# Optimization experiments

Measured on AMD Instinct MI355X. Metric: run time of the kernel, lower is better.

Reference implementation:

```python
import jax, jax.numpy as jnp
import numpy as np

EPS = 1e-8
BETA = 0.05
K = 8192
D = 256
M = 32768


def _l2_normalize(x, axis=-1):
    # matches torch F.normalize: x / max(||x||, eps)
    n = jnp.linalg.norm(x, axis=axis, keepdims=True)
    return x / jnp.maximum(n, EPS)


def setup_inputs() -> dict:
    key = jax.random.key(0)
    kz, ke = jax.random.split(key)
    z = jax.random.normal(kz, (M, D), dtype=jnp.float32)
    # codebook initialized as unit-norm rows, as in the torch __init__
    E = _l2_normalize(jax.random.normal(ke, (K, D), dtype=jnp.float32), axis=1)
    return {"z": z, "E": E}


def reference(z, E):
    z_flat = z.reshape(-1, z.shape[-1])          # [M, D]
    z_n = _l2_normalize(z_flat, axis=1)          # [M, D]
    E_n = _l2_normalize(E, axis=1)               # [K, D]
    sims = jnp.einsum('md,kd->mk', z_n, E_n)     # [M, K] cosine similarity
    idx = jnp.argmax(sims, axis=1)               # [M]
    zq = E[idx]                                  # [M, D] gather
    zq_n = _l2_normalize(zq, axis=1)
    commit = jnp.mean((jax.lax.stop_gradient(zq_n) - z_n) ** 2)
    codebk = jnp.mean((zq_n - jax.lax.stop_gradient(z_n)) ** 2)
    loss = commit + BETA * codebk
    zq_st = z_flat + jax.lax.stop_gradient(zq - z_flat)  # straight-through
    return loss, zq_st, idx
```

## Files before the change

kernel.cpp:

```cpp
#include <hip/hip_runtime.h>
#include <float.h>
#include <math.h>
#include <stdint.h>

#define M_ROWS 32768
#define K_CODES 8192
#define DDIM 256
#define BM 64
#define BN 64
#define NTILES (K_CODES / BN)
#define DELTA 0.009f
#define CAP 16
#define FLAGBIT 0x10000

typedef __attribute__((ext_vector_type(8))) short short8;
typedef __attribute__((ext_vector_type(4))) float f32x4;

__device__ inline unsigned short f2bf(float f) {
    unsigned u = __float_as_uint(f);
    return (unsigned short)((u + 0x7fffu + ((u >> 16) & 1u)) >> 16);
}
__device__ inline unsigned fkey(float f) {
    unsigned u = __float_as_uint(f);
    return u ^ ((unsigned)((int)u >> 31) | 0x80000000u);
}
__device__ inline float fkey_inv(unsigned k) {
    unsigned u = (k & 0x80000000u) ? (k ^ 0x80000000u) : ~k;
    return __uint_as_float(u);
}

#define GLOAD16(gsrc, ldst)                                                     \
    __builtin_amdgcn_global_load_lds(                                           \
        (const __attribute__((address_space(1))) void*)(gsrc),                  \
        (__attribute__((address_space(3))) void*)(ldst), 16, 0, 0)

__global__ __launch_bounds__(256) void k_norm_E(const float* __restrict__ E,
                                                float* __restrict__ En,
                                                unsigned short* __restrict__ En_b) {
    int wid  = threadIdx.x >> 6;
    int lane = threadIdx.x & 63;
    int row  = blockIdx.x * 4 + wid;
    const float* e = E + (size_t)row * DDIM;
    float v[4];
    float ssq = 0.f;
#pragma unroll
    for (int p = 0; p < 4; ++p) { v[p] = e[lane + 64 * p]; ssq += v[p] * v[p]; }
#pragma unroll
    for (int off = 32; off >= 1; off >>= 1) ssq += __shfl_xor(ssq, off);
    float inv = 1.f / fmaxf(sqrtf(ssq), 1e-8f);
    float* o = En + (size_t)row * DDIM;
    unsigned short* ob = En_b + (size_t)row * DDIM;
#pragma unroll
    for (int p = 0; p < 4; ++p) {
        float nv = v[p] * inv;
        o[lane + 64 * p]  = nv;
        ob[lane + 64 * p] = f2bf(nv);
    }
}

__global__ __launch_bounds__(256, 2) void k_cand(
    const float* __restrict__ z,
    const unsigned short* __restrict__ En_b,
    unsigned char* __restrict__ cand_cnt,
    int* __restrict__ cand_k) {

    __shared__ __attribute__((aligned(16))) char smem[65536];
    unsigned* rowmaxKey = (unsigned*)smem;
    int*      cnt       = (int*)(smem + 256);
    int*      list      = (int*)(smem + 512);

    const int tid  = threadIdx.x;
    const int lane = tid & 63;
    const int wid  = tid >> 6;
    const int lo   = lane & 15;
    const int hi   = lane >> 4;
    const int m0   = blockIdx.x * BM;

    const char* eb = (const char*)En_b;
    char* b0 = smem + wid * 16384;
    char* b1 = smem + wid * 16384 + 8192;

    int sofs[8];
#pragma unroll
    for (int i = 0; i < 8; ++i) {
        int G   = i * 64 + lane;
        int row = G >> 5;
        int g   = (G & 31) ^ (row & 7);
        sofs[i] = (wid * 16 + row) * 512 + g * 16;
    }

    auto stage = [&](int ktile, char* bufp) {
        const char* tb = eb + (size_t)ktile * (BN * 512);
#pragma unroll
        for (int i = 0; i < 8; ++i)
            GLOAD16(tb + sofs[i], bufp + i * 1024);
    };

    stage(0, b0);
    stage(1, b1);

    short8 af[4][8];
#pragma unroll
    for (int mi = 0; mi < 4; ++mi) {
        const float* zr = z + (size_t)(m0 + mi * 16 + lo) * DDIM;
        float ssq = 0.f;
#pragma unroll
        for (int ks = 0; ks < 8; ++ks) {
            int e0 = (ks * 4 + hi) * 8;
            float4 a = *(const float4*)&zr[e0];
            float4 b = *(const float4*)&zr[e0 + 4];
            ssq += a.x * a.x + a.y * a.y + a.z * a.z + a.w * a.w;
            ssq += b.x * b.x + b.y * b.y + b.z * b.z + b.w * b.w;
        }
        ssq += __shfl_xor(ssq, 16);
        ssq += __shfl_xor(ssq, 32);
        float inv = 1.f / fmaxf(sqrtf(ssq), 1e-8f);
        const float* zr2 = zr;
        asm volatile("" : "+v"(zr2));
#pragma unroll
        for (int ks = 0; ks < 8; ++ks) {
            int e0 = (ks * 4 + hi) * 8;
            float4 a = *(const float4*)&zr2[e0];
            float4 b = *(const float4*)&zr2[e0 + 4];
            short8 s8;
            s8[0] = (short)f2bf(a.x * inv); s8[1] = (short)f2bf(a.y * inv);
            s8[2] = (short)f2bf(a.z * inv); s8[3] = (short)f2bf(a.w * inv);
            s8[4] = (short)f2bf(b.x * inv); s8[5] = (short)f2bf(b.y * inv);
            s8[6] = (short)f2bf(b.z * inv); s8[7] = (short)f2bf(b.w * inv);
            af[mi][ks] = s8;
        }
    }

    float v1[16], v2[16];
    int   k1[16];
#pragma unroll
    for (int s = 0; s < 16; ++s) { v1[s] = -FLT_MAX; v2[s] = -FLT_MAX; k1[s] = 0; }

    __syncthreads();

    const int bswz = lo & 7;

    for (int t = 0; t < NTILES; ++t) {
        if (t < NTILES - 1) asm volatile("s_waitcnt vmcnt(8)" ::: "memory");
        else                asm volatile("s_waitcnt vmcnt(0)" ::: "memory");
        __builtin_amdgcn_sched_barrier(0);

        const unsigned short* Bc = (const unsigned short*)((t & 1) ? b1 : b0);
        f32x4 acc[4];
#pragma unroll
        for (int mi = 0; mi < 4; ++mi) acc[mi] = (f32x4){0.f, 0.f, 0.f, 0.f};
#pragma unroll
        for (int ks = 0; ks < 8; ++ks) {
            short8 bf = *(const short8*)&Bc[lo * 256 + (((ks * 4 + hi) ^ bswz)) * 8];
#pragma unroll
            for (int mi = 0; mi < 4; ++mi)
                acc[mi] = __builtin_amdgcn_mfma_f32_16x16x32_bf16(af[mi][ks], bf, acc[mi], 0, 0, 0);
        }

        const int kv = t * BN + wid * 16 + lo;
#pragma unroll
        for (int mi = 0; mi < 4; ++mi)
#pragma unroll
            for (int r = 0; r < 4; ++r) {
                int s = mi * 4 + r;
                float v = acc[mi][r];
                v2[s] = fmaxf(v2[s], fminf(v1[s], v));
                k1[s] = (v > v1[s]) ? kv : k1[s];
                v1[s] = fmaxf(v1[s], v);
            }

        if (t + 2 < NTILES) {
            asm volatile("s_waitcnt lgkmcnt(0)" ::: "memory");
            __builtin_amdgcn_sched_barrier(0);
            stage(t + 2, (t & 1) ? b1 : b0);
        }
    }

    __syncthreads();
    if (tid < BM) { cnt[tid] = 0; rowmaxKey[tid] = 0u; }
    __syncthreads();

#pragma unroll
    for (int s = 0; s < 16; ++s) {
        float w = v1[s];
        w = fmaxf(w, __shfl_xor(w, 1));
        w = fmaxf(w, __shfl_xor(w, 2));
        w = fmaxf(w, __shfl_xor(w, 4));
        w = fmaxf(w, __shfl_xor(w, 8));
        if (lo == 0) {
            int row = (s >> 2) * 16 + hi * 4 + (s & 3);
            atomicMax(&rowmaxKey[row], fkey(w));
        }
    }
    __syncthreads();

#pragma unroll
    for (int s = 0; s < 16; ++s) {
        int row = (s >> 2) * 16 + hi * 4 + (s & 3);
        float thr = fkey_inv(rowmaxKey[row]) - DELTA;
        if (v1[s] >= thr) {
            int pos = atomicAdd(&cnt[row], 1);
            if (pos < CAP) list[row * CAP + pos] = k1[s];
        }
        if (v2[s] >= thr) {
            int pos = atomicAdd(&cnt[row], 1);
            if (pos < CAP) list[row * CAP + pos] = FLAGBIT | (wid * 16 + lo);
        }
    }
    __syncthreads();

    if (tid < BM) {
        int c = cnt[tid];
        cand_cnt[m0 + tid] = (unsigned char)(c > CAP ? 255 : c);
        int n = c < CAP ? c : CAP;
        for (int j = 0; j < n; ++j) cand_k[(size_t)(m0 + tid) * CAP + j] = list[tid * CAP + j];
    }
}

__global__ __launch_bounds__(256) void k_final(
    const float* __restrict__ z,
    const float* __restrict__ E,
    const float* __restrict__ En,
    const unsigned char* __restrict__ cand_cnt,
    const int* __restrict__ cand_k,
    float* __restrict__ out,
    float* __restrict__ rowloss) {

    __shared__ float zl[4][256];
    int wid  = threadIdx.x >> 6;
    int lane = threadIdx.x & 63;
    int m    = blockIdx.x * 4 + wid;

    const float* zr = z + (size_t)m * DDIM;
    const float4 zz = *(const float4*)&zr[lane * 4];
    *(float4*)&zl[wid][lane * 4] = zz;
    asm volatile("s_waitcnt lgkmcnt(0)" ::: "memory");

    float bv = -FLT_MAX;
    int   bk = 0x7fffffff;

    auto rescan = [&](int cb) {
#pragma unroll
        for (int j = 0; j < 2; ++j) {
            int k = cb + (lane * 2 + j) * 64;
            const float4* er = (const float4*)&En[(size_t)k * DDIM];
            float s0 = 0.f, s1 = 0.f, s2 = 0.f, s3 = 0.f;
#pragma unroll 16
            for (int d4 = 0; d4 < 64; ++d4) {
                float4 e  = er[d4];
                float4 zd = *(const float4*)&zl[wid][d4 * 4];
                s0 += zd.x * e.x; s1 += zd.y * e.y;
                s2 += zd.z * e.z; s3 += zd.w * e.w;
            }
            float s = (s0 + s1) + (s2 + s3);
            if (s > bv || (s == bv && k < bk)) { bv = s; bk = k; }
        }
    };

    int c = cand_cnt[m];
    if (c != 255) {
        for (int j = 0; j < c; ++j) {
            int e = cand_k[(size_t)m * CAP + j];
            if (e < FLAGBIT) {
                const float4 ee = *(const float4*)&En[(size_t)e * DDIM + lane * 4];
                float s = zz.x * ee.x + zz.y * ee.y + zz.z * ee.z + zz.w * ee.w;
#pragma unroll
                for (int off = 1; off < 64; off <<= 1) s += __shfl_xor(s, off);
                if (s > bv || (s == bv && e < bk)) { bv = s; bk = e; }
            } else {
                rescan(e & 63);
            }
        }
    } else {
        for (int cb = 0; cb < 64; ++cb) rescan(cb);
    }
#pragma unroll
    for (int off = 1; off < 64; off <<= 1) {
        float ov = __shfl_xor(bv, off);
        int   ok = __shfl_xor(bk, off);
        if (ov > bv || (ov == bv && ok < bk)) { bv = ov; bk = ok; }
    }
    const int idx = bk;

    const float* er = E + (size_t)idx * DDIM;
    float zv[4], ev[4];
    float sz = 0.f, se = 0.f;
#pragma unroll
    for (int p = 0; p < 4; ++p) {
        zv[p] = zr[lane + 64 * p]; sz += zv[p] * zv[p];
        ev[p] = er[lane + 64 * p]; se += ev[p] * ev[p];
    }
#pragma unroll
    for (int off = 32; off >= 1; off >>= 1) {
        sz += __shfl_xor(sz, off);
        se += __shfl_xor(se, off);
    }
    float nz = fmaxf(sqrtf(sz), 1e-8f);
    float ne = fmaxf(sqrtf(se), 1e-8f);

    float rs = 0.f;
    float* zq = out + 1 + (size_t)m * DDIM;
#pragma unroll
    for (int p = 0; p < 4; ++p) {
        float zn = zv[p] / nz;
        float en = ev[p] / ne;
        float d  = en - zn;
        rs += d * d;
        zq[lane + 64 * p] = zv[p] + (ev[p] - zv[p]);
    }
#pragma unroll
    for (int off = 32; off >= 1; off >>= 1) rs += __shfl_xor(rs, off);

    if (lane == 0) {
        rowloss[m] = rs;
        out[1 + (size_t)M_ROWS * DDIM + m] = (float)idx;
    }
}

__global__ __launch_bounds__(256) void k_loss(const float* __restrict__ rowloss,
                                              float* __restrict__ out) {
    __shared__ double sm[256];
    double s = 0.0;
    for (int i = threadIdx.x; i < M_ROWS; i += 256) s += (double)rowloss[i];
    sm[threadIdx.x] = s;
    __syncthreads();
    for (int st = 128; st > 0; st >>= 1) {
        if (threadIdx.x < st) sm[threadIdx.x] += sm[threadIdx.x + st];
        __syncthreads();
    }
    if (threadIdx.x == 0) {
        float c = (float)(sm[0] / (double)((size_t)M_ROWS * DDIM));
        out[0] = c + 0.05f * c;
    }
}

extern "C" void kernel_launch(void* const* d_in, const int* in_sizes, int n_in,
                              void* d_out, int out_size, void* d_ws, size_t ws_size,
                              hipStream_t stream) {
    const float* z = (const float*)d_in[0];
    const float* E = (const float*)d_in[1];
    float* out = (float*)d_out;

    char* ws = (char*)d_ws;
    size_t off = 0;
    float*          En       = (float*)(ws + off);          off += (size_t)K_CODES * DDIM * 4;
    unsigned short* En_b     = (unsigned short*)(ws + off); off += (size_t)K_CODES * DDIM * 2;
    int*            cand_k   = (int*)(ws + off);            off += (size_t)M_ROWS * CAP * 4;
    unsigned char*  cand_cnt = (unsigned char*)(ws + off);  off += (size_t)M_ROWS;
    float*          rowloss  = (float*)(ws + off);

    k_norm_E<<<K_CODES / 4, 256, 0, stream>>>(E, En, En_b);
    k_cand<<<M_ROWS / BM, 256, 0, stream>>>(z, En_b, cand_cnt, cand_k);
    k_final<<<M_ROWS / 4, 256, 0, stream>>>(z, E, En, cand_cnt, cand_k, out, rowloss);
    k_loss<<<1, 256, 0, stream>>>(rowloss, out);
}
```

Before: 299.6 us.

## Replace top-2 candidate tracking with two-pass max-then-threshold scan

The candidate kernel now runs the bf16 MFMA similarity sweep twice. The first pass tracks only per-row maxima, and the second recomputes all tiles and appends every code within DELTA of the row max to a global list using global atomics. This removes the per-tile top-2 and index bookkeeping and the costly fallback rescans of whole 64-code columns in the final kernel. In exchange it doubles the GEMM work in k_cand, adds a memset and global atomics, and falls back to a full fp32 scan when a row overflows CAP.

```diff
diff --git a/kernel.cpp b/kernel.cpp
--- a/kernel.cpp
+++ b/kernel.cpp
@@ -11,7 +11,6 @@
 #define NTILES (K_CODES / BN)
 #define DELTA 0.009f
 #define CAP 16
-#define FLAGBIT 0x10000
 
 typedef __attribute__((ext_vector_type(8))) short short8;
 typedef __attribute__((ext_vector_type(4))) float f32x4;
@@ -61,13 +60,10 @@
 __global__ __launch_bounds__(256, 2) void k_cand(
     const float* __restrict__ z,
     const unsigned short* __restrict__ En_b,
-    unsigned char* __restrict__ cand_cnt,
+    int* __restrict__ cntG,
     int* __restrict__ cand_k) {
 
     __shared__ __attribute__((aligned(16))) char smem[65536];
-    unsigned* rowmaxKey = (unsigned*)smem;
-    int*      cnt       = (int*)(smem + 256);
-    int*      list      = (int*)(smem + 512);
 
     const int tid  = threadIdx.x;
     const int lane = tid & 63;
@@ -131,14 +127,13 @@
         }
     }
 
-    float v1[16], v2[16];
-    int   k1[16];
-#pragma unroll
-    for (int s = 0; s < 16; ++s) { v1[s] = -FLT_MAX; v2[s] = -FLT_MAX; k1[s] = 0; }
-
-    __syncthreads();
-
     const int bswz = lo & 7;
+
+    float pmax[16];
+#pragma unroll
+    for (int s = 0; s < 16; ++s) pmax[s] = -FLT_MAX;
+
+    __syncthreads();
 
     for (int t = 0; t < NTILES; ++t) {
         if (t < NTILES - 1) asm volatile("s_waitcnt vmcnt(8)" ::: "memory");
@@ -156,18 +151,11 @@
             for (int mi = 0; mi < 4; ++mi)
                 acc[mi] = __builtin_amdgcn_mfma_f32_16x16x32_bf16(af[mi][ks], bf, acc[mi], 0, 0, 0);
         }
-
-        const int kv = t * BN + wid * 16 + lo;
 #pragma unroll
         for (int mi = 0; mi < 4; ++mi)
 #pragma unroll
-            for (int r = 0; r < 4; ++r) {
-                int s = mi * 4 + r;
-                float v = acc[mi][r];
-                v2[s] = fmaxf(v2[s], fminf(v1[s], v));
-                k1[s] = (v > v1[s]) ? kv : k1[s];
-                v1[s] = fmaxf(v1[s], v);
-            }
+            for (int r = 0; r < 4; ++r)
+                pmax[mi * 4 + r] = fmaxf(pmax[mi * 4 + r], acc[mi][r]);
 
         if (t + 2 < NTILES) {
             asm volatile("s_waitcnt lgkmcnt(0)" ::: "memory");
@@ -177,12 +165,12 @@
     }
 
     __syncthreads();
-    if (tid < BM) { cnt[tid] = 0; rowmaxKey[tid] = 0u; }
-    __syncthreads();
-
+    unsigned* rowmaxKey = (unsigned*)smem;
+    if (tid < BM) rowmaxKey[tid] = 0u;
+    __syncthreads();
 #pragma unroll
     for (int s = 0; s < 16; ++s) {
-        float w = v1[s];
+        float w = pmax[s];
         w = fmaxf(w, __shfl_xor(w, 1));
         w = fmaxf(w, __shfl_xor(w, 2));
         w = fmaxf(w, __shfl_xor(w, 4));
@@ -193,27 +181,51 @@
         }
     }
     __syncthreads();
-
+    float thr[16];
 #pragma unroll
     for (int s = 0; s < 16; ++s) {
         int row = (s >> 2) * 16 + hi * 4 + (s & 3);
-        float thr = fkey_inv(rowmaxKey[row]) - DELTA;
-        if (v1[s] >= thr) {
-            int pos = atomicAdd(&cnt[row], 1);
-            if (pos < CAP) list[row * CAP + pos] = k1[s];
-        }
-        if (v2[s] >= thr) {
-            int pos = atomicAdd(&cnt[row], 1);
-            if (pos < CAP) list[row * CAP + pos] = FLAGBIT | (wid * 16 + lo);
-        }
-    }
-    __syncthreads();
-
-    if (tid < BM) {
-        int c = cnt[tid];
-        cand_cnt[m0 + tid] = (unsigned char)(c > CAP ? 255 : c);
-        int n = c < CAP ? c : CAP;
-        for (int j = 0; j < n; ++j) cand_k[(size_t)(m0 + tid) * CAP + j] = list[tid * CAP + j];
+        thr[s] = fkey_inv(rowmaxKey[row]) - DELTA;
+    }
+    __syncthreads();
+
+    stage(0, b0);
+    stage(1, b1);
+
+    for (int t = 0; t < NTILES; ++t) {
+        if (t < NTILES - 1) asm volatile("s_waitcnt vmcnt(8)" ::: "memory");
+        else                asm volatile("s_waitcnt vmcnt(0)" ::: "memory");
+        __builtin_amdgcn_sched_barrier(0);
+
+        const unsigned short* Bc = (const unsigned short*)((t & 1) ? b1 : b0);
+        f32x4 acc[4];
+#pragma unroll
+        for (int mi = 0; mi < 4; ++mi) acc[mi] = (f32x4){0.f, 0.f, 0.f, 0.f};
+#pragma unroll
+        for (int ks = 0; ks < 8; ++ks) {
+            short8 bf = *(const short8*)&Bc[lo * 256 + (((ks * 4 + hi) ^ bswz)) * 8];
+#pragma unroll
+            for (int mi = 0; mi < 4; ++mi)
+                acc[mi] = __builtin_amdgcn_mfma_f32_16x16x32_bf16(af[mi][ks], bf, acc[mi], 0, 0, 0);
+        }
+
+        const int kv = t * BN + wid * 16 + lo;
+#pragma unroll
+        for (int mi = 0; mi < 4; ++mi)
+#pragma unroll
+            for (int r = 0; r < 4; ++r) {
+                if (acc[mi][r] >= thr[mi * 4 + r]) {
+                    int m = m0 + mi * 16 + hi * 4 + r;
+                    int pos = atomicAdd(&cntG[m], 1);
+                    if (pos < CAP) cand_k[(size_t)m * CAP + pos] = kv;
+                }
+            }
+
+        if (t + 2 < NTILES) {
+            asm volatile("s_waitcnt lgkmcnt(0)" ::: "memory");
+            __builtin_amdgcn_sched_barrier(0);
+            stage(t + 2, (t & 1) ? b1 : b0);
+        }
     }
 }
 
@@ -221,7 +233,7 @@
     const float* __restrict__ z,
     const float* __restrict__ E,
     const float* __restrict__ En,
-    const unsigned char* __restrict__ cand_cnt,
+    const int* __restrict__ cntG,
     const int* __restrict__ cand_k,
     float* __restrict__ out,
     float* __restrict__ rowloss) {
@@ -239,13 +251,22 @@
     float bv = -FLT_MAX;
     int   bk = 0x7fffffff;
 
-    auto rescan = [&](int cb) {
-#pragma unroll
-        for (int j = 0; j < 2; ++j) {
-            int k = cb + (lane * 2 + j) * 64;
+    int c = cntG[m];
+    if (c <= CAP) {
+        for (int j = 0; j < c; ++j) {
+            int k = cand_k[(size_t)m * CAP + j];
+            const float4 ee = *(const float4*)&En[(size_t)k * DDIM + lane * 4];
+            float s = zz.x * ee.x + zz.y * ee.y + zz.z * ee.z + zz.w * ee.w;
+#pragma unroll
+            for (int off = 1; off < 64; off <<= 1) s += __shfl_xor(s, off);
+            if (s > bv || (s == bv && k < bk)) { bv = s; bk = k; }
+        }
+    } else {
+        for (int kb = 0; kb < K_CODES; kb += 64) {
+            int k = kb + lane;
             const float4* er = (const float4*)&En[(size_t)k * DDIM];
             float s0 = 0.f, s1 = 0.f, s2 = 0.f, s3 = 0.f;
-#pragma unroll 16
+#pragma unroll 8
             for (int d4 = 0; d4 < 64; ++d4) {
                 float4 e  = er[d4];
                 float4 zd = *(const float4*)&zl[wid][d4 * 4];
@@ -255,24 +276,6 @@
             float s = (s0 + s1) + (s2 + s3);
             if (s > bv || (s == bv && k < bk)) { bv = s; bk = k; }
         }
-    };
-
-    int c = cand_cnt[m];
-    if (c != 255) {
-        for (int j = 0; j < c; ++j) {
-            int e = cand_k[(size_t)m * CAP + j];
-            if (e < FLAGBIT) {
-                const float4 ee = *(const float4*)&En[(size_t)e * DDIM + lane * 4];
-                float s = zz.x * ee.x + zz.y * ee.y + zz.z * ee.z + zz.w * ee.w;
-#pragma unroll
-                for (int off = 1; off < 64; off <<= 1) s += __shfl_xor(s, off);
-                if (s > bv || (s == bv && e < bk)) { bv = s; bk = e; }
-            } else {
-                rescan(e & 63);
-            }
-        }
-    } else {
-        for (int cb = 0; cb < 64; ++cb) rescan(cb);
     }
 #pragma unroll
     for (int off = 1; off < 64; off <<= 1) {
@@ -343,14 +346,15 @@
 
     char* ws = (char*)d_ws;
     size_t off = 0;
-    float*          En       = (float*)(ws + off);          off += (size_t)K_CODES * DDIM * 4;
-    unsigned short* En_b     = (unsigned short*)(ws + off); off += (size_t)K_CODES * DDIM * 2;
-    int*            cand_k   = (int*)(ws + off);            off += (size_t)M_ROWS * CAP * 4;
-    unsigned char*  cand_cnt = (unsigned char*)(ws + off);  off += (size_t)M_ROWS;
-    float*          rowloss  = (float*)(ws + off);
-
+    float*          En      = (float*)(ws + off);          off += (size_t)K_CODES * DDIM * 4;
+    unsigned short* En_b    = (unsigned short*)(ws + off); off += (size_t)K_CODES * DDIM * 2;
+    int*            cand_k  = (int*)(ws + off);            off += (size_t)M_ROWS * CAP * 4;
+    int*            cntG    = (int*)(ws + off);            off += (size_t)M_ROWS * 4;
+    float*          rowloss = (float*)(ws + off);
+
+    hipMemsetAsync(cntG, 0, (size_t)M_ROWS * 4, stream);
     k_norm_E<<<K_CODES / 4, 256, 0, stream>>>(E, En, En_b);
-    k_cand<<<M_ROWS / BM, 256, 0, stream>>>(z, En_b, cand_cnt, cand_k);
-    k_final<<<M_ROWS / 4, 256, 0, stream>>>(z, E, En, cand_cnt, cand_k, out, rowloss);
+    k_cand<<<M_ROWS / BM, 256, 0, stream>>>(z, En_b, cntG, cand_k);
+    k_final<<<M_ROWS / 4, 256, 0, stream>>>(z, E, En, cntG, cand_k, out, rowloss);
     k_loss<<<1, 256, 0, stream>>>(rowloss, out);
 }
```

New measurement: 378.4 us. 26.3% more time.

## Fuse candidate refinement and output epilogue into the candidate kernel

Applied to the files above, without the earlier changes.

Merges k_final into k_cand, so each wave re-ranks its 16 rows' candidates straight from shared memory and then writes zq, idx and the row loss. This drops the global candidate list round trip and one kernel launch. In exchange each wave handles 16 rows one after another inside a kernel limited to 2 blocks per SM, which lowers parallelism for the latency-bound gather and rescan work. It also reuses part of the wave's tile buffer as the z staging area.

```diff
diff --git a/kernel.cpp b/kernel.cpp
--- a/kernel.cpp
+++ b/kernel.cpp
@@ -60,9 +60,11 @@
 
 __global__ __launch_bounds__(256, 2) void k_cand(
     const float* __restrict__ z,
+    const float* __restrict__ E,
+    const float* __restrict__ En,
     const unsigned short* __restrict__ En_b,
-    unsigned char* __restrict__ cand_cnt,
-    int* __restrict__ cand_k) {
+    float* __restrict__ out,
+    float* __restrict__ rowloss) {
 
     __shared__ __attribute__((aligned(16))) char smem[65536];
     unsigned* rowmaxKey = (unsigned*)smem;
@@ -209,111 +211,94 @@
     }
     __syncthreads();
 
-    if (tid < BM) {
-        int c = cnt[tid];
-        cand_cnt[m0 + tid] = (unsigned char)(c > CAP ? 255 : c);
-        int n = c < CAP ? c : CAP;
-        for (int j = 0; j < n; ++j) cand_k[(size_t)(m0 + tid) * CAP + j] = list[tid * CAP + j];
-    }
-}
-
-__global__ __launch_bounds__(256) void k_final(
-    const float* __restrict__ z,
-    const float* __restrict__ E,
-    const float* __restrict__ En,
-    const unsigned char* __restrict__ cand_cnt,
-    const int* __restrict__ cand_k,
-    float* __restrict__ out,
-    float* __restrict__ rowloss) {
-
-    __shared__ float zl[4][256];
-    int wid  = threadIdx.x >> 6;
-    int lane = threadIdx.x & 63;
-    int m    = blockIdx.x * 4 + wid;
-
-    const float* zr = z + (size_t)m * DDIM;
-    const float4 zz = *(const float4*)&zr[lane * 4];
-    *(float4*)&zl[wid][lane * 4] = zz;
-    asm volatile("s_waitcnt lgkmcnt(0)" ::: "memory");
-
-    float bv = -FLT_MAX;
-    int   bk = 0x7fffffff;
-
-    auto rescan = [&](int cb) {
-#pragma unroll
-        for (int j = 0; j < 2; ++j) {
-            int k = cb + (lane * 2 + j) * 64;
-            const float4* er = (const float4*)&En[(size_t)k * DDIM];
-            float s0 = 0.f, s1 = 0.f, s2 = 0.f, s3 = 0.f;
+    float* zl = (float*)(smem + wid * 16384 + 8192);
+    for (int rr = 0; rr < 16; ++rr) {
+        const int row = wid * 16 + rr;
+        const int m   = m0 + row;
+        const float* zr = z + (size_t)m * DDIM;
+        const float4 zz = *(const float4*)&zr[lane * 4];
+        *(float4*)&zl[lane * 4] = zz;
+        asm volatile("s_waitcnt lgkmcnt(0)" ::: "memory");
+
+        float bv = -FLT_MAX;
+        int   bk = 0x7fffffff;
+
+        auto rescan = [&](int cb) {
+#pragma unroll
+            for (int j = 0; j < 2; ++j) {
+                int k = cb + (lane * 2 + j) * 64;
+                const float4* er4 = (const float4*)&En[(size_t)k * DDIM];
+                float s0 = 0.f, s1 = 0.f, s2 = 0.f, s3 = 0.f;
 #pragma unroll 16
-            for (int d4 = 0; d4 < 64; ++d4) {
-                float4 e  = er[d4];
-                float4 zd = *(const float4*)&zl[wid][d4 * 4];
-                s0 += zd.x * e.x; s1 += zd.y * e.y;
-                s2 += zd.z * e.z; s3 += zd.w * e.w;
+                for (int d4 = 0; d4 < 64; ++d4) {
+                    float4 e  = er4[d4];
+                    float4 zd = *(const float4*)&zl[d4 * 4];
+                    s0 += zd.x * e.x; s1 += zd.y * e.y;
+                    s2 += zd.z * e.z; s3 += zd.w * e.w;
+                }
+                float s = (s0 + s1) + (s2 + s3);
+                if (s > bv || (s == bv && k < bk)) { bv = s; bk = k; }
             }
-            float s = (s0 + s1) + (s2 + s3);
-            if (s > bv || (s == bv && k < bk)) { bv = s; bk = k; }
-        }
-    };
-
-    int c = cand_cnt[m];
-    if (c != 255) {
-        for (int j = 0; j < c; ++j) {
-            int e = cand_k[(size_t)m * CAP + j];
-            if (e < FLAGBIT) {
-                const float4 ee = *(const float4*)&En[(size_t)e * DDIM + lane * 4];
-                float s = zz.x * ee.x + zz.y * ee.y + zz.z * ee.z + zz.w * ee.w;
-#pragma unroll
-                for (int off = 1; off < 64; off <<= 1) s += __shfl_xor(s, off);
-                if (s > bv || (s == bv && e < bk)) { bv = s; bk = e; }
-            } else {
-                rescan(e & 63);
+        };
+
+        int c = cnt[row];
+        if (c <= CAP) {
+            for (int j = 0; j < c; ++j) {
+                int e = list[row * CAP + j];
+                if (e < FLAGBIT) {
+                    const float4 ee = *(const float4*)&En[(size_t)e * DDIM + lane * 4];
+                    float s = zz.x * ee.x + zz.y * ee.y + zz.z * ee.z + zz.w * ee.w;
+#pragma unroll
+                    for (int off = 1; off < 64; off <<= 1) s += __shfl_xor(s, off);
+                    if (s > bv || (s == bv && e < bk)) { bv = s; bk = e; }
+                } else {
+                    rescan(e & 63);
+                }
             }
-        }
-    } else {
-        for (int cb = 0; cb < 64; ++cb) rescan(cb);
-    }
-#pragma unroll
-    for (int off = 1; off < 64; off <<= 1) {
-        float ov = __shfl_xor(bv, off);
-        int   ok = __shfl_xor(bk, off);
-        if (ov > bv || (ov == bv && ok < bk)) { bv = ov; bk = ok; }
-    }
-    const int idx = bk;
-
-    const float* er = E + (size_t)idx * DDIM;
-    float zv[4], ev[4];
-    float sz = 0.f, se = 0.f;
-#pragma unroll
-    for (int p = 0; p < 4; ++p) {
-        zv[p] = zr[lane + 64 * p]; sz += zv[p] * zv[p];
-        ev[p] = er[lane + 64 * p]; se += ev[p] * ev[p];
-    }
-#pragma unroll
-    for (int off = 32; off >= 1; off >>= 1) {
-        sz += __shfl_xor(sz, off);
-        se += __shfl_xor(se, off);
-    }
-    float nz = fmaxf(sqrtf(sz), 1e-8f);
-    float ne = fmaxf(sqrtf(se), 1e-8f);
-
-    float rs = 0.f;
-    float* zq = out + 1 + (size_t)m * DDIM;
-#pragma unroll
-    for (int p = 0; p < 4; ++p) {
-        float zn = zv[p] / nz;
-        float en = ev[p] / ne;
-        float d  = en - zn;
-        rs += d * d;
-        zq[lane + 64 * p] = zv[p] + (ev[p] - zv[p]);
-    }
-#pragma unroll
-    for (int off = 32; off >= 1; off >>= 1) rs += __shfl_xor(rs, off);
-
-    if (lane == 0) {
-        rowloss[m] = rs;
-        out[1 + (size_t)M_ROWS * DDIM + m] = (float)idx;
+        } else {
+            for (int cb = 0; cb < 64; ++cb) rescan(cb);
+        }
+#pragma unroll
+        for (int off = 1; off < 64; off <<= 1) {
+            float ov = __shfl_xor(bv, off);
+            int   ok = __shfl_xor(bk, off);
+            if (ov > bv || (ov == bv && ok < bk)) { bv = ov; bk = ok; }
+        }
+        const int idx = bk;
+
+        const float* er = E + (size_t)idx * DDIM;
+        float zv[4], ev[4];
+        float sz = 0.f, se = 0.f;
+#pragma unroll
+        for (int p = 0; p < 4; ++p) {
+            zv[p] = zr[lane + 64 * p]; sz += zv[p] * zv[p];
+            ev[p] = er[lane + 64 * p]; se += ev[p] * ev[p];
+        }
+#pragma unroll
+        for (int off = 32; off >= 1; off >>= 1) {
+            sz += __shfl_xor(sz, off);
+            se += __shfl_xor(se, off);
+        }
+        float nz = fmaxf(sqrtf(sz), 1e-8f);
+        float ne = fmaxf(sqrtf(se), 1e-8f);
+
+        float rs = 0.f;
+        float* zq = out + 1 + (size_t)m * DDIM;
+#pragma unroll
+        for (int p = 0; p < 4; ++p) {
+            float zn = zv[p] / nz;
+            float en = ev[p] / ne;
+            float d  = en - zn;
+            rs += d * d;
+            zq[lane + 64 * p] = zv[p] + (ev[p] - zv[p]);
+        }
+#pragma unroll
+        for (int off = 32; off >= 1; off >>= 1) rs += __shfl_xor(rs, off);
+
+        if (lane == 0) {
+            rowloss[m] = rs;
+            out[1 + (size_t)M_ROWS * DDIM + m] = (float)idx;
+        }
     }
 }
 
@@ -343,14 +328,11 @@
 
     char* ws = (char*)d_ws;
     size_t off = 0;
-    float*          En       = (float*)(ws + off);          off += (size_t)K_CODES * DDIM * 4;
-    unsigned short* En_b     = (unsigned short*)(ws + off); off += (size_t)K_CODES * DDIM * 2;
-    int*            cand_k   = (int*)(ws + off);            off += (size_t)M_ROWS * CAP * 4;
-    unsigned char*  cand_cnt = (unsigned char*)(ws + off);  off += (size_t)M_ROWS;
-    float*          rowloss  = (float*)(ws + off);
+    float*          En      = (float*)(ws + off);          off += (size_t)K_CODES * DDIM * 4;
+    unsigned short* En_b    = (unsigned short*)(ws + off); off += (size_t)K_CODES * DDIM * 2;
+    float*          rowloss = (float*)(ws + off);
 
     k_norm_E<<<K_CODES / 4, 256, 0, stream>>>(E, En, En_b);
-    k_cand<<<M_ROWS / BM, 256, 0, stream>>>(z, En_b, cand_cnt, cand_k);
-    k_final<<<M_ROWS / 4, 256, 0, stream>>>(z, E, En, cand_cnt, cand_k, out, rowloss);
+    k_cand<<<M_ROWS / BM, 256, 0, stream>>>(z, E, En, En_b, out, rowloss);
     k_loss<<<1, 256, 0, stream>>>(rowloss, out);
 }
```

Result: slower. 311.2 us (+3.8%).
